# Kernel tuning notes

Hardware: AMD Instinct MI355X
Metric: run time of the kernel (lower is better)

The kernel has to match this reference:

```python
import jax, jax.numpy as jnp
import numpy as np

B, T, DIN, D = 32, 2048, 512, 512


def setup_inputs() -> dict:
    key = jax.random.key(0)
    k0, k1, k2, k3 = jax.random.split(key, 4)
    x = jax.random.normal(k0, (B, T, DIN), dtype=jnp.float32)
    h0 = jax.random.normal(k1, (B, D), dtype=jnp.float32)
    s0 = jax.random.normal(k2, (B, D), dtype=jnp.float32)
    # nn.Linear(input_dim, 6*hidden_dim): weight [6D, DIN], bias [6D]
    W = jax.random.normal(k3, (6 * D, DIN), dtype=jnp.float32) / np.float32(np.sqrt(DIN))
    b = jnp.zeros((6 * D,), dtype=jnp.float32)
    return {"x": x, "h0": h0, "s0": s0, "W": W, "b": b}


def reference(x, h0, s0, W, b):
    # Fused input projection for all 6 gates, done once as a big GEMM: [B,T,6D]
    proj = jnp.einsum("bti,oi->bto", x, W) + b
    proj = jnp.transpose(proj, (1, 0, 2))  # [T, B, 6D] for scan over time
    sig = jax.nn.sigmoid

    def step(carry, z):
        h, s = carry  # each [B, D]
        z0, z1, z2, z3, z4, z5 = jnp.split(z, 6, axis=-1)
        # gated two-state recurrence (6 gates, input-only projection,
        # elementwise recurrence on h/s as in the fused Triton cell)
        s_new = sig(z0) * s + sig(z1) * jnp.tanh(z2)
        h_new = sig(z3) * h + sig(z4) * jnp.tanh(z5 + s_new)
        return (h_new, s_new), h_new

    (hT, sT), hs = jax.lax.scan(step, (h0, s0), proj)
    out = jnp.transpose(hs, (1, 0, 2))  # [B, T, D]
    return out, sT
```

## Files before the change

### kernel.cpp

```cpp
#include <hip/hip_runtime.h>
#include <hip/hip_bf16.h>
#include <cstddef>
#include <cstdint>

#define BB   32
#define TT   2048
#define DIN  512
#define DD   512
#define NN   3072
#define PW   3072
#define PF   16
#define SCANBLKS 32

#define BMT 256
#define BNT 256
#define BKT 32
#define NKT (DIN / BKT)

typedef __attribute__((ext_vector_type(4))) float f32x4;
typedef __attribute__((ext_vector_type(8))) short s16x8;

__device__ __forceinline__ void gl2lds16(const void* g, void* l) {
    __builtin_amdgcn_global_load_lds(
        (const __attribute__((address_space(1))) unsigned*)g,
        (__attribute__((address_space(3))) unsigned*)l, 16, 0, 0);
}

__device__ __forceinline__ unsigned short bfr(float f) {
    unsigned u = __float_as_uint(f);
    u += 0x7fffu + ((u >> 16) & 1u);
    return (unsigned short)(u >> 16);
}

__device__ __forceinline__ float ftanh(float x) {
    return 1.f - 2.f * __builtin_amdgcn_rcpf(1.f + __builtin_amdgcn_exp2f(x * 2.885390082f));
}

__device__ __forceinline__ float h2lo(unsigned u) {
    return (float)__builtin_bit_cast(_Float16, (unsigned short)(u & 0xffffu));
}
__device__ __forceinline__ float h2hi(unsigned u) {
    return (float)__builtin_bit_cast(_Float16, (unsigned short)(u >> 16));
}

__global__ __launch_bounds__(256) void convert_x(
    const float* __restrict__ x, unsigned short* __restrict__ x2)
{
    const int total4 = BB * TT * DIN / 4;
    for (int idx = blockIdx.x * 256 + threadIdx.x; idx < total4;
         idx += gridDim.x * 256) {
        int e = idx * 4;
        int b = e >> 20;
        int t = (e >> 9) & 2047;
        int i = e & 511;
        float4 v = *(const float4*)(x + (size_t)e);
        ushort4 o;
        o.x = bfr(v.x); o.y = bfr(v.y); o.z = bfr(v.z); o.w = bfr(v.w);
        *(ushort4*)(x2 + ((size_t)((t << 5) | b) << 9) + i) = o;
    }
}

__global__ __launch_bounds__(128) void convert_w(
    const float* __restrict__ W, const float* __restrict__ bias,
    unsigned short* __restrict__ W2, float* __restrict__ bias2)
{
    int c = blockIdx.x;
    int p = c >> 10, d = (c & 1023) >> 1, q = c & 1;
    int o = ((2 * p + q) << 9) + d;
    const float* src = W + (size_t)o * DIN;
    unsigned short* dst = W2 + (size_t)c * DIN;
    int i = threadIdx.x * 4;
    float4 v = *(const float4*)(src + i);
    ushort4 u;
    u.x = bfr(v.x); u.y = bfr(v.y); u.z = bfr(v.z); u.w = bfr(v.w);
    *(ushort4*)(dst + i) = u;
    if (threadIdx.x == 0) bias2[c] = bias[o];
}

__global__ __launch_bounds__(512, 2) void fused_chunk(
    const unsigned short* __restrict__ x2,
    const unsigned short* __restrict__ W2,
    const float* __restrict__ bias2,
    _Float16* __restrict__ projDst,
    const _Float16* __restrict__ projSrc,
    const float* __restrict__ h0, const float* __restrict__ s0,
    float* __restrict__ outH, float* __restrict__ outS,
    int t0g, int Tcg, int t0s, int Tcs)
{
    __shared__ unsigned short lds[3 * 16384];

    if (blockIdx.x < SCANBLKS) {
        if (t0s < 0) return;
        const int gid = blockIdx.x * 512 + threadIdx.x;
        const int b   = gid >> 9;
        const int d   = gid & 511;

        float h, s;
        if (t0s == 0) { h = h0[gid]; s = s0[gid]; }
        else {
            h = outH[((size_t)b * TT + (t0s - 1)) * DD + d];
            s = outS[gid];
        }

        const unsigned* pu = (const unsigned*)(projSrc + (size_t)b * PW + d * 2);
        const size_t tstr = (size_t)BB * PW / 2;
        float* oH = outH + ((size_t)b * TT + t0s) * DD + d;

        unsigned bufA[PF][3], bufB[PF][3];
        #pragma unroll
        for (int u = 0; u < PF; ++u)
            #pragma unroll
            for (int p = 0; p < 3; ++p)
                bufA[u][p] = pu[(size_t)u * tstr + p * 512];

        for (int tb = 0; tb < Tcs; tb += 2 * PF) {
            #pragma unroll
            for (int u = 0; u < PF; ++u) {
                int t = tb + PF + u; if (t > Tcs - 1) t = Tcs - 1;
                #pragma unroll
                for (int p = 0; p < 3; ++p)
                    bufB[u][p] = pu[(size_t)t * tstr + p * 512];
            }
            #pragma unroll
            for (int u = 0; u < PF; ++u) {
                float a0 = h2lo(bufA[u][0]), a1 = h2hi(bufA[u][0]);
                float t2 = h2lo(bufA[u][1]), a3 = h2hi(bufA[u][1]);
                float a4 = h2lo(bufA[u][2]), z5 = h2hi(bufA[u][2]);
                s = __builtin_fmaf(a0, s, a1 * t2);
                h = __builtin_fmaf(a3, h, a4 * ftanh(z5 + s));
                oH[(size_t)(tb + u) * DD] = h;
            }
            #pragma unroll
            for (int u = 0; u < PF; ++u) {
                int t = tb + 2 * PF + u; if (t > Tcs - 1) t = Tcs - 1;
                #pragma unroll
                for (int p = 0; p < 3; ++p)
                    bufA[u][p] = pu[(size_t)t * tstr + p * 512];
            }
            #pragma unroll
            for (int u = 0; u < PF; ++u) {
                float a0 = h2lo(bufB[u][0]), a1 = h2hi(bufB[u][0]);
                float t2 = h2lo(bufB[u][1]), a3 = h2hi(bufB[u][1]);
                float a4 = h2lo(bufB[u][2]), z5 = h2hi(bufB[u][2]);
                s = __builtin_fmaf(a0, s, a1 * t2);
                h = __builtin_fmaf(a3, h, a4 * ftanh(z5 + s));
                oH[(size_t)(tb + PF + u) * DD] = h;
            }
        }
        outS[gid] = s;
        return;
    }

    if (t0g < 0) return;
    const unsigned nwg = gridDim.x - SCANBLKS;
    const unsigned fb  = blockIdx.x - SCANBLKS;
    const unsigned qq  = nwg >> 3, rr8 = nwg & 7;
    const unsigned xcd = fb & 7, sid = fb >> 3;
    const unsigned work = (xcd < rr8 ? xcd * (qq + 1)
                                     : rr8 * (qq + 1) + (xcd - rr8) * qq) + sid;
    const int bx = (int)(work % (NN / BNT));
    const int by = (int)(work / (NN / BNT));

    const int tid  = threadIdx.x;
    const int row0 = by * BMT;
    const int col0 = bx * BNT;
    const size_t growA = (size_t)t0g * BB + row0;

    const int lane = tid & 63;
    const int wv   = tid >> 6;
    const int wm   = wv >> 2;
    const int wn   = wv & 3;
    const int lr   = lane & 15;
    const int lq   = lane >> 4;

    auto stageA = [&](int s, int kt) {
        unsigned short* Ab = lds + s * 16384;
        const int k0 = kt * BKT;
        #pragma unroll
        for (int a = 0; a < 2; ++a) {
            int cid = a * 512 + tid;
            int rt  = cid >> 2;
            int cp  = cid & 3;
            gl2lds16(x2 + (growA + rt) * DIN + k0 + cp * 8, Ab + cid * 8);
        }
    };
    auto stageB = [&](int s, int kt) {
        unsigned short* Bb = lds + s * 16384 + 8192;
        const int k0 = kt * BKT;
        #pragma unroll
        for (int a = 0; a < 2; ++a) {
            int cid = a * 512 + tid;
            int rt  = cid >> 2;
            int cp  = cid & 3;
            gl2lds16(W2 + (size_t)(col0 + rt) * DIN + k0 + cp * 8, Bb + cid * 8);
        }
    };

    f32x4 acc[8][4] = {};

    stageA(0, 0); stageB(0, 0);
    stageA(1, 1); stageB(1, 1);
    asm volatile("s_waitcnt vmcnt(4)" ::: "memory");
    __builtin_amdgcn_s_barrier();

    #pragma unroll
    for (int kt = 0; kt < NKT; ++kt) {
        const unsigned short* Ab = lds + (kt % 3) * 16384;
        const unsigned short* Bb = Ab + 8192;
        const bool st = (kt + 2) < NKT;

        if (st) { stageA((kt + 2) % 3, kt + 2); stageB((kt + 2) % 3, kt + 2); }

        s16x8 bv[4], av[8];
        #pragma unroll
        for (int j = 0; j < 4; ++j) {
            int col = wn * 64 + j * 16 + lr;
            bv[j] = *(const s16x8*)(Bb + col * BKT + lq * 8);
        }
        #pragma unroll
        for (int m = 0; m < 8; ++m) {
            int row = wm * 128 + m * 16 + lr;
            av[m] = *(const s16x8*)(Ab + row * BKT + lq * 8);
        }

        __builtin_amdgcn_s_setprio(1);
        #pragma unroll
        for (int m = 0; m < 8; ++m)
            #pragma unroll
            for (int j = 0; j < 4; ++j)
                acc[m][j] = __builtin_amdgcn_mfma_f32_16x16x32_bf16(
                    bv[j], av[m], acc[m][j], 0, 0, 0);
        __builtin_amdgcn_s_setprio(0);

        if (kt + 1 < NKT) {
            if (st) asm volatile("s_waitcnt vmcnt(4)" ::: "memory");
            else    asm volatile("s_waitcnt vmcnt(0)" ::: "memory");
            __builtin_amdgcn_s_barrier();
        }
    }

    const int p = col0 >> 10;
    const bool evenTanh = (p == 1);
    const bool oddIdent = (p == 2);
    const float mEven = evenTanh ? 2.885390082f : -1.442695041f;

    char* epi = (char*)lds + 32768 + wv * 2304;
    const int colw = col0 + wn * 64;
    const int l8 = lane & 7, lh = lane >> 3;

    #pragma unroll
    for (int m = 0; m < 8; ++m) {
        #pragma unroll
        for (int j = 0; j < 4; ++j) {
            float4 bc = *(const float4*)(bias2 + colw + j * 16 + lq * 4);
            float z0 = acc[m][j][0] + bc.x;
            float z1 = acc[m][j][1] + bc.y;
            float z2 = acc[m][j][2] + bc.z;
            float z3 = acc[m][j][3] + bc.w;
            float e0 = __builtin_amdgcn_rcpf(1.f + __builtin_amdgcn_exp2f(z0 * mEven));
            float e2 = __builtin_amdgcn_rcpf(1.f + __builtin_amdgcn_exp2f(z2 * mEven));
            float v0 = evenTanh ? (1.f - 2.f * e0) : e0;
            float v2 = evenTanh ? (1.f - 2.f * e2) : e2;
            float v1 = oddIdent ? z1
                : __builtin_amdgcn_rcpf(1.f + __builtin_amdgcn_exp2f(z1 * -1.442695041f));
            float v3 = oddIdent ? z3
                : __builtin_amdgcn_rcpf(1.f + __builtin_amdgcn_exp2f(z3 * -1.442695041f));
            ushort4 o;
            o.x = __builtin_bit_cast(unsigned short, (_Float16)v0);
            o.y = __builtin_bit_cast(unsigned short, (_Float16)v1);
            o.z = __builtin_bit_cast(unsigned short, (_Float16)v2);
            o.w = __builtin_bit_cast(unsigned short, (_Float16)v3);
            *(ushort4*)(epi + lr * 144 + j * 32 + lq * 8) = o;
        }
        #pragma unroll
        for (int hh = 0; hh < 2; ++hh) {
            int rr = hh * 8 + lh;
            uint4 v = *(const uint4*)(epi + rr * 144 + l8 * 16);
            int g = row0 + wm * 128 + m * 16 + rr;
            *(uint4*)((char*)projDst + ((size_t)g * PW + colw + l8 * 8) * 2) = v;
        }
    }
}

extern "C" void kernel_launch(void* const* d_in, const int* in_sizes, int n_in,
                              void* d_out, int out_size, void* d_ws, size_t ws_size,
                              hipStream_t stream) {
    const float* x    = (const float*)d_in[0];
    const float* h0   = (const float*)d_in[1];
    const float* s0   = (const float*)d_in[2];
    const float* W    = (const float*)d_in[3];
    const float* bias = (const float*)d_in[4];

    float* outH = (float*)d_out;
    float* outS = outH + (size_t)BB * TT * DD;

    char* ws = (char*)d_ws;
    const size_t x2_bytes = (size_t)BB * TT * DIN * 2;
    const size_t w2_bytes = (size_t)NN * DIN * 2;
    const size_t b2_bytes = (size_t)NN * 4;
    unsigned short* x2    = (unsigned short*)ws;
    unsigned short* W2    = (unsigned short*)(ws + x2_bytes);
    float*          bias2 = (float*)(ws + x2_bytes + w2_bytes);

    const size_t fixed = x2_bytes + w2_bytes + b2_bytes;
    const size_t per_t = (size_t)BB * PW * 2;
    size_t avail = ws_size > fixed ? ws_size - fixed : 0;
    int TcMax = (int)(avail / (2 * per_t));
    if (TcMax > 512) TcMax = 512;
    TcMax &= ~31;
    if (TcMax < 32) TcMax = 32;

    _Float16* projA = (_Float16*)(ws + fixed);
    _Float16* projB = projA + (size_t)TcMax * BB * PW;

    convert_x<<<2048, 256, 0, stream>>>(x, x2);
    convert_w<<<NN, 128, 0, stream>>>(W, bias, W2, bias2);

    const int nC = (TT + TcMax - 1) / TcMax;
    int prevT0 = -1, prevTc = 0;
    const _Float16* prevProj = nullptr;

    for (int ci = 0; ci <= nC; ++ci) {
        const bool hasG = (ci < nC);
        int t0 = ci * TcMax;
        int Tc = 0;
        _Float16* dst = nullptr;
        int nG = 0;
        if (hasG) {
            Tc  = TT - t0; if (Tc > TcMax) Tc = TcMax;
            dst = (ci & 1) ? projB : projA;
            nG  = (NN / BNT) * (Tc * BB / BMT);
        }
        fused_chunk<<<dim3(SCANBLKS + nG), 512, 0, stream>>>(
            x2, W2, bias2, dst, prevProj, h0, s0, outH, outS,
            hasG ? t0 : -1, Tc, prevT0, prevTc);
        if (hasG) { prevProj = dst; prevT0 = t0; prevTc = Tc; }
    }
}
```

Before: 461.1 us.

## Overlap x bf16 conversion of next chunk with GEMM and scan blocks

Replaces the upfront full-tensor x conversion with a per-chunk conversion: only the first chunk is converted before the loop, and 48 extra blocks inside each fused_chunk launch convert the next chunk's slice while the GEMM and scan blocks run. The chunk schedule is also changed so the last chunk is shortened, which shrinks the non-overlapped tail scan. This is meant to hide the conversion cost behind compute. The extra blocks compete with the GEMM for bandwidth and compute units, and the conversion reads x with a strided pattern.

Result: slower. 475.4 us (+3.1%).

```diff
diff --git a/kernel.cpp b/kernel.cpp
--- a/kernel.cpp
+++ b/kernel.cpp
@@ -11,6 +11,7 @@
 #define PW   3072
 #define PF   16
 #define SCANBLKS 32
+#define CONVB    48
 
 #define BMT 256
 #define BNT 256
@@ -43,20 +44,21 @@
     return (float)__builtin_bit_cast(_Float16, (unsigned short)(u >> 16));
 }
 
-__global__ __launch_bounds__(256) void convert_x(
-    const float* __restrict__ x, unsigned short* __restrict__ x2)
+__global__ __launch_bounds__(256) void convert_x_slice(
+    const float* __restrict__ x, unsigned short* __restrict__ x2,
+    int ts, int Tcs)
 {
-    const int total4 = BB * TT * DIN / 4;
-    for (int idx = blockIdx.x * 256 + threadIdx.x; idx < total4;
+    const int total = Tcs * BB * (DIN / 4);
+    for (int idx = blockIdx.x * 256 + threadIdx.x; idx < total;
          idx += gridDim.x * 256) {
-        int e = idx * 4;
-        int b = e >> 20;
-        int t = (e >> 9) & 2047;
-        int i = e & 511;
-        float4 v = *(const float4*)(x + (size_t)e);
+        int r2 = idx >> 7;
+        int i4 = idx & 127;
+        int lt = r2 >> 5, b = r2 & 31;
+        int t  = ts + lt;
+        float4 v = *(const float4*)(x + ((size_t)b * TT + t) * DIN + i4 * 4);
         ushort4 o;
         o.x = bfr(v.x); o.y = bfr(v.y); o.z = bfr(v.z); o.w = bfr(v.w);
-        *(ushort4*)(x2 + ((size_t)((t << 5) | b) << 9) + i) = o;
+        *(ushort4*)(x2 + (((size_t)((t << 5) | b)) << 9) + i4 * 4) = o;
     }
 }
 
@@ -78,6 +80,7 @@
 }
 
 __global__ __launch_bounds__(512, 2) void fused_chunk(
+    const float* __restrict__ x,
     const unsigned short* __restrict__ x2,
     const unsigned short* __restrict__ W2,
     const float* __restrict__ bias2,
@@ -85,7 +88,7 @@
     const _Float16* __restrict__ projSrc,
     const float* __restrict__ h0, const float* __restrict__ s0,
     float* __restrict__ outH, float* __restrict__ outS,
-    int t0g, int Tcg, int t0s, int Tcs)
+    int t0g, int Tcg, int t0s, int Tcs, int tC, int TcC)
 {
     __shared__ unsigned short lds[3 * 16384];
 
@@ -151,9 +154,26 @@
         return;
     }
 
+    if (blockIdx.x < SCANBLKS + CONVB) {
+        if (tC < 0) return;
+        const int total = TcC * BB * (DIN / 4);
+        for (int idx = (blockIdx.x - SCANBLKS) * 512 + threadIdx.x; idx < total;
+             idx += CONVB * 512) {
+            int r2 = idx >> 7;
+            int i4 = idx & 127;
+            int lt = r2 >> 5, b = r2 & 31;
+            int t  = tC + lt;
+            float4 v = *(const float4*)(x + ((size_t)b * TT + t) * DIN + i4 * 4);
+            ushort4 o;
+            o.x = bfr(v.x); o.y = bfr(v.y); o.z = bfr(v.z); o.w = bfr(v.w);
+            *(ushort4*)((unsigned short*)x2 + (((size_t)((t << 5) | b)) << 9) + i4 * 4) = o;
+        }
+        return;
+    }
+
     if (t0g < 0) return;
-    const unsigned nwg = gridDim.x - SCANBLKS;
-    const unsigned fb  = blockIdx.x - SCANBLKS;
+    const unsigned nwg = gridDim.x - SCANBLKS - CONVB;
+    const unsigned fb  = blockIdx.x - SCANBLKS - CONVB;
     const unsigned qq  = nwg >> 3, rr8 = nwg & 7;
     const unsigned xcd = fb & 7, sid = fb >> 3;
     const unsigned work = (xcd < rr8 ? xcd * (qq + 1)
@@ -313,27 +333,36 @@
     _Float16* projA = (_Float16*)(ws + fixed);
     _Float16* projB = projA + (size_t)TcMax * BB * PW;
 
-    convert_x<<<2048, 256, 0, stream>>>(x, x2);
+    int sch_t0[80], sch_Tc[80], nC = 0;
+    {
+        int t0 = 0;
+        while (t0 < TT && nC < 80) {
+            int rem = TT - t0;
+            int Tc = TcMax < rem ? TcMax : rem;
+            if (Tc == rem && Tc > 160) Tc -= 128;
+            sch_t0[nC] = t0; sch_Tc[nC] = Tc; ++nC; t0 += Tc;
+        }
+    }
+
     convert_w<<<NN, 128, 0, stream>>>(W, bias, W2, bias2);
-
-    const int nC = (TT + TcMax - 1) / TcMax;
+    convert_x_slice<<<512, 256, 0, stream>>>(x, x2, sch_t0[0], sch_Tc[0]);
+
     int prevT0 = -1, prevTc = 0;
     const _Float16* prevProj = nullptr;
 
     for (int ci = 0; ci <= nC; ++ci) {
         const bool hasG = (ci < nC);
-        int t0 = ci * TcMax;
-        int Tc = 0;
+        int t0 = 0, Tc = 0, tC = -1, TcC = 0, nG = 0;
         _Float16* dst = nullptr;
-        int nG = 0;
         if (hasG) {
-            Tc  = TT - t0; if (Tc > TcMax) Tc = TcMax;
+            t0  = sch_t0[ci]; Tc = sch_Tc[ci];
             dst = (ci & 1) ? projB : projA;
             nG  = (NN / BNT) * (Tc * BB / BMT);
-        }
-        fused_chunk<<<dim3(SCANBLKS + nG), 512, 0, stream>>>(
-            x2, W2, bias2, dst, prevProj, h0, s0, outH, outS,
-            hasG ? t0 : -1, Tc, prevT0, prevTc);
+            if (ci + 1 < nC) { tC = sch_t0[ci + 1]; TcC = sch_Tc[ci + 1]; }
+        }
+        fused_chunk<<<dim3(SCANBLKS + CONVB + nG), 512, 0, stream>>>(
+            x, x2, W2, bias2, dst, prevProj, h0, s0, outH, outS,
+            hasG ? t0 : -1, Tc, prevT0, prevTc, tC, TcC);
         if (hasG) { prevProj = dst; prevT0 = t0; prevTc = Tc; }
     }
 }
```
